# Optimization experiments

Hardware: AMD Instinct MI355X
Metric: run time of the kernel (lower is better)

The kernel has to match this reference:

```python
import jax, jax.numpy as jnp
import numpy as np

D_MODEL = 1024
NHEAD = 16
HEAD_DIM = D_MODEL // NHEAD
D_FF = 4096
B, S = 2, 2048
LN_EPS = 1e-5


def _linear_params(key, d_out, d_in):
    kw, kb = jax.random.split(key)
    lim = 1.0 / np.sqrt(d_in)
    W = jax.random.uniform(kw, (d_out, d_in), jnp.float32, -lim, lim)
    b = jax.random.uniform(kb, (d_out,), jnp.float32, -lim, lim)
    return W, b


def setup_inputs() -> dict:
    key = jax.random.key(0)
    ks = jax.random.split(key, 8)
    src = jax.random.normal(ks[0], (B, S, D_MODEL), jnp.float32)
    mask = jax.random.randint(ks[1], (B, S), 0, 2).astype(bool)
    Wq, bq = _linear_params(ks[2], D_MODEL, D_MODEL)
    Wk, bk = _linear_params(ks[3], D_MODEL, D_MODEL)
    Wv, bv = _linear_params(ks[4], D_MODEL, D_MODEL)
    Wo, bo = _linear_params(ks[5], D_MODEL, D_MODEL)
    W1, b1 = _linear_params(ks[6], D_FF, D_MODEL)
    W2, b2 = _linear_params(ks[7], D_MODEL, D_FF)
    ln1_g = jnp.ones((D_MODEL,), jnp.float32)
    ln1_b = jnp.zeros((D_MODEL,), jnp.float32)
    ln2_g = jnp.ones((D_MODEL,), jnp.float32)
    ln2_b = jnp.zeros((D_MODEL,), jnp.float32)
    return dict(src=src, mask=mask, Wq=Wq, bq=bq, Wk=Wk, bk=bk, Wv=Wv, bv=bv,
                Wo=Wo, bo=bo, W1=W1, b1=b1, W2=W2, b2=b2,
                ln1_g=ln1_g, ln1_b=ln1_b, ln2_g=ln2_g, ln2_b=ln2_b)


def _layernorm(x, g, b):
    mu = jnp.mean(x, axis=-1, keepdims=True)
    var = jnp.mean(jnp.square(x - mu), axis=-1, keepdims=True)
    return (x - mu) * jax.lax.rsqrt(var + LN_EPS) * g + b


def reference(src, mask, Wq, bq, Wk, bk, Wv, bv, Wo, bo, W1, b1, W2, b2,
              ln1_g, ln1_b, ln2_g, ln2_b):
    batch, seq, _ = src.shape
    src_norm = _layernorm(src, ln1_g, ln1_b)
    # projections (torch Linear: x @ W.T + b), split heads -> [B,H,S,Dh]
    def proj(W, b):
        y = jnp.einsum('bsi,oi->bso', src_norm, W) + b
        return y.reshape(batch, seq, NHEAD, HEAD_DIM).transpose(0, 2, 1, 3)
    q, k, v = proj(Wq, bq), proj(Wk, bk), proj(Wv, bv)
    scores = jnp.einsum('bhqd,bhkd->bhqk', q, k) / np.sqrt(HEAD_DIM)
    scores = jnp.where(mask[:, None, None, :], -10000.0, scores)
    attn_probs = jax.nn.softmax(scores, axis=-1)
    attn_out = jnp.einsum('bhqk,bhkd->bhqd', attn_probs, v)
    attn_out = attn_out.transpose(0, 2, 1, 3).reshape(batch, seq, D_MODEL)
    attn_out = jnp.einsum('bsi,oi->bso', attn_out, Wo) + bo
    src = src + attn_out
    src_norm2 = _layernorm(src, ln2_g, ln2_b)
    h = jax.nn.relu(jnp.einsum('bsi,oi->bso', src_norm2, W1) + b1)
    ff = jnp.einsum('bsi,oi->bso', h, W2) + b2
    src = src + ff
    return (src, attn_probs)
```

## Files before the change

### kernel.cpp

```cpp
#include <hip/hip_runtime.h>
#include <math.h>

typedef __bf16 bf16;
typedef __bf16 bf16x4 __attribute__((ext_vector_type(4)));
typedef __bf16 bf16x8 __attribute__((ext_vector_type(8)));
typedef float f32x4 __attribute__((ext_vector_type(4)));

__device__ __forceinline__ f32x4 mfma16(bf16x8 a, bf16x8 b, f32x4 c) {
  return __builtin_amdgcn_mfma_f32_16x16x32_bf16(a, b, c, 0, 0, 0);
}

__device__ __forceinline__ void gload_lds16(const void* g, void* l) {
  __builtin_amdgcn_global_load_lds((__attribute__((address_space(1))) void*)(g),
                                   (__attribute__((address_space(3))) void*)(l),
                                   16, 0, 0);
}

__global__ __launch_bounds__(256)
void cvt_all(const float* __restrict__ Wq, const float* __restrict__ Wk,
             const float* __restrict__ Wv, const float* __restrict__ Wo,
             const float* __restrict__ W1, const float* __restrict__ W2,
             const float* __restrict__ bq, const float* __restrict__ bk,
             const float* __restrict__ bv, bf16* __restrict__ wqkv,
             bf16* __restrict__ wob, bf16* __restrict__ w1b,
             bf16* __restrict__ w2b, float* __restrict__ bqkv) {
  const int i = blockIdx.x * 256 + threadIdx.x;
  if (i < 3145728) {
    float4 v;
    bf16* dst;
    size_t di;
    if (i < 262144) { v = ((const float4*)Wq)[i]; dst = wqkv; di = i; }
    else if (i < 524288) { v = ((const float4*)Wk)[i - 262144]; dst = wqkv; di = i; }
    else if (i < 786432) { v = ((const float4*)Wv)[i - 524288]; dst = wqkv; di = i; }
    else if (i < 1048576) { v = ((const float4*)Wo)[i - 786432]; dst = wob; di = i - 786432; }
    else if (i < 2097152) { v = ((const float4*)W1)[i - 1048576]; dst = w1b; di = i - 1048576; }
    else { v = ((const float4*)W2)[i - 2097152]; dst = w2b; di = i - 2097152; }
    bf16x4 o;
    o[0] = (bf16)v.x; o[1] = (bf16)v.y; o[2] = (bf16)v.z; o[3] = (bf16)v.w;
    reinterpret_cast<bf16x4*>(dst)[di] = o;
  } else {
    const int j = i - 3145728;
    const float* s = (j < 256) ? bq : ((j < 512) ? bk : bv);
    reinterpret_cast<float4*>(bqkv)[j] = reinterpret_cast<const float4*>(s)[j & 255];
  }
}

__global__ __launch_bounds__(256)
void ln_bf16(const float* __restrict__ x, const float* __restrict__ g,
             const float* __restrict__ bta, bf16* __restrict__ y) {
  const int row = blockIdx.x, t = threadIdx.x;
  const float4 v = reinterpret_cast<const float4*>(x)[(size_t)row * 256 + t];
  float s1 = v.x + v.y + v.z + v.w;
  float s2 = v.x * v.x + v.y * v.y + v.z * v.z + v.w * v.w;
#pragma unroll
  for (int m = 1; m < 64; m <<= 1) {
    s1 += __shfl_xor(s1, m);
    s2 += __shfl_xor(s2, m);
  }
  __shared__ float red[8];
  if ((t & 63) == 0) { red[(t >> 6) * 2] = s1; red[(t >> 6) * 2 + 1] = s2; }
  __syncthreads();
  s1 = red[0] + red[2] + red[4] + red[6];
  s2 = red[1] + red[3] + red[5] + red[7];
  const float mu = s1 * (1.f / 1024.f);
  const float rs = rsqrtf(s2 * (1.f / 1024.f) - mu * mu + 1e-5f);
  const float4 gv = reinterpret_cast<const float4*>(g)[t];
  const float4 bv = reinterpret_cast<const float4*>(bta)[t];
  bf16x4 o;
  o[0] = (bf16)((v.x - mu) * rs * gv.x + bv.x);
  o[1] = (bf16)((v.y - mu) * rs * gv.y + bv.y);
  o[2] = (bf16)((v.z - mu) * rs * gv.z + bv.z);
  o[3] = (bf16)((v.w - mu) * rs * gv.w + bv.w);
  reinterpret_cast<bf16x4*>(y)[(size_t)row * 256 + t] = o;
}

__global__ __launch_bounds__(256)
void tr_v(const bf16* __restrict__ QKV, bf16* __restrict__ VT) {
  __shared__ bf16 T[64 * 80];
  const int t = threadIdx.x;
  const int sb = blockIdx.x * 64, h = blockIdx.y, b = blockIdx.z;
  const int srow = t >> 2, c16 = t & 3;
  const bf16* src = QKV + (size_t)(b * 2048 + sb + srow) * 3072 + 2048 + h * 64 + c16 * 16;
  bf16x8 a0 = *reinterpret_cast<const bf16x8*>(src);
  bf16x8 a1 = *reinterpret_cast<const bf16x8*>(src + 8);
  *reinterpret_cast<bf16x8*>(&T[srow * 80 + c16 * 16]) = a0;
  *reinterpret_cast<bf16x8*>(&T[srow * 80 + c16 * 16 + 8]) = a1;
  __syncthreads();
  const int drow = t >> 2, sq = t & 3;
  bf16x8 o0, o1;
#pragma unroll
  for (int j = 0; j < 8; ++j) o0[j] = T[(sq * 16 + j) * 80 + drow];
#pragma unroll
  for (int j = 0; j < 8; ++j) o1[j] = T[(sq * 16 + 8 + j) * 80 + drow];
  bf16* dst = VT + ((size_t)(b * 16 + h) * 64 + drow) * 2048 + sb + sq * 16;
  *reinterpret_cast<bf16x8*>(dst) = o0;
  *reinterpret_cast<bf16x8*>(dst + 8) = o1;
}

template <bool OUT_BF16, bool RELU, bool RES, bool QSC>
__global__ __launch_bounds__(256)
void gemm_bt(const bf16* __restrict__ A, const bf16* __restrict__ Bw,
             const float* __restrict__ bias, const float* __restrict__ res,
             void* __restrict__ Cout, int M, int N, int K) {
  __shared__ bf16 As[3][128 * 32];
  __shared__ bf16 Bs[3][128 * 32];
  const int t = threadIdx.x, wave = t >> 6, lane = t & 63;
  const int l15 = lane & 15, lhi = lane >> 4;
  const int nwg = gridDim.x * gridDim.y;
  const int orig = blockIdx.y * gridDim.x + blockIdx.x;
  const int wgid = (orig & 7) * (nwg >> 3) + (orig >> 3);
  const int bx = wgid % gridDim.x, by = wgid / gridDim.x;
  const int m0 = by * 128, n0 = bx * 128;
  const int wm = (wave >> 1) * 64, wn = (wave & 1) * 64;
  const f32x4 z4 = {0.f, 0.f, 0.f, 0.f};
  f32x4 acc[4][4];
#pragma unroll
  for (int m = 0; m < 4; ++m)
#pragma unroll
    for (int n = 0; n < 4; ++n) acc[m][n] = z4;

  const int soff0 = wave * 1024 + lane * 16;
  const int soff1 = (4 + wave) * 1024 + lane * 16;
  const int srow0 = soff0 >> 6, scol0 = (soff0 & 63) >> 1;
  const int srow1 = soff1 >> 6, scol1 = (soff1 & 63) >> 1;

#define GEMM_STAGE(k0, bb)                                                    \
  do {                                                                        \
    gload_lds16(A + (size_t)(m0 + srow0) * K + (k0) + scol0,                  \
                (char*)As[bb] + soff0);                                       \
    gload_lds16(Bw + (size_t)(n0 + srow0) * K + (k0) + scol0,                 \
                (char*)Bs[bb] + soff0);                                       \
    gload_lds16(A + (size_t)(m0 + srow1) * K + (k0) + scol1,                  \
                (char*)As[bb] + soff1);                                       \
    gload_lds16(Bw + (size_t)(n0 + srow1) * K + (k0) + scol1,                 \
                (char*)Bs[bb] + soff1);                                       \
  } while (0)

  const int nt = K >> 5;
  GEMM_STAGE(0, 0);
  GEMM_STAGE(32, 1);
  asm volatile("s_waitcnt vmcnt(4)" ::: "memory");
  __builtin_amdgcn_s_barrier();

  for (int kt = 0; kt < nt; ++kt) {
    if (kt + 2 < nt) GEMM_STAGE((kt + 2) * 32, (kt + 2) % 3);
    const bf16* Ac = As[kt % 3];
    const bf16* Bc = Bs[kt % 3];
    bf16x8 af[4], bfr[4];
#pragma unroll
    for (int m = 0; m < 4; ++m)
      af[m] = *reinterpret_cast<const bf16x8*>(&Ac[(wm + m * 16 + l15) * 32 + lhi * 8]);
#pragma unroll
    for (int n = 0; n < 4; ++n)
      bfr[n] = *reinterpret_cast<const bf16x8*>(&Bc[(wn + n * 16 + l15) * 32 + lhi * 8]);
    __builtin_amdgcn_s_setprio(1);
#pragma unroll
    for (int m = 0; m < 4; ++m)
#pragma unroll
      for (int n = 0; n < 4; ++n) acc[m][n] = mfma16(af[m], bfr[n], acc[m][n]);
    __builtin_amdgcn_s_setprio(0);
    if (kt + 1 < nt) {
      if (kt + 2 < nt)
        asm volatile("s_waitcnt vmcnt(4)" ::: "memory");
      else
        asm volatile("s_waitcnt vmcnt(0)" ::: "memory");
      __builtin_amdgcn_s_barrier();
    }
  }
#undef GEMM_STAGE

  const float sc = (QSC && n0 < 1024) ? 0.125f : 1.0f;
#pragma unroll
  for (int m = 0; m < 4; ++m) {
    const int row_base = m0 + wm + m * 16 + lhi * 4;
#pragma unroll
    for (int n = 0; n < 4; ++n) {
      const int col = n0 + wn + n * 16 + l15;
      const float bv = bias[col];
#pragma unroll
      for (int r = 0; r < 4; ++r) {
        const int row = row_base + r;
        float v = (acc[m][n][r] + bv) * sc;
        if (RELU) v = v > 0.f ? v : 0.f;
        if (RES) v += res[(size_t)row * N + col];
        if (OUT_BF16)
          ((bf16*)Cout)[(size_t)row * N + col] = (bf16)v;
        else
          ((float*)Cout)[(size_t)row * N + col] = v;
      }
    }
  }
}

__global__ __launch_bounds__(512)
void attn_fused2(const bf16* __restrict__ Qp, const bf16* __restrict__ Kp,
                 const bf16* __restrict__ VTp, const int* __restrict__ mask,
                 float* __restrict__ probs, bf16* __restrict__ Ob) {
  constexpr int S = 2048, LD = 3072, KB = 128, NT = S / KB;
  __shared__ bf16 Kt[KB * 64];
  __shared__ bf16 Vt[64 * KB];
  __shared__ bf16 P[128 * KB];
  __shared__ float msk2[2][KB];
  const int t = threadIdx.x, wave = t >> 6, lane = t & 63;
  const int l15 = lane & 15, lhi = lane >> 4;
  const int flat = blockIdx.x + 16 * (blockIdx.y + 16 * blockIdx.z);
  const int wg = (flat & 7) * 64 + (flat >> 3);
  const int q0 = (wg & 15) * 128, h = (wg >> 4) & 15, b = wg >> 8;
  const int* mrow = mask + b * S;
  const f32x4 z4 = {0.f, 0.f, 0.f, 0.f};

  const bf16* kgp[2];
  const bf16* vgp[2];
  int soff[2];
#pragma unroll
  for (int i = 0; i < 2; ++i) {
    const int off = (i * 8 + wave) * 1024 + lane * 16;
    soff[i] = off;
    const int krow = off >> 7, kbin = off & 127;
    kgp[i] = Kp + (size_t)(b * S + krow) * LD + h * 64 + ((kbin ^ ((krow & 7) << 4)) >> 1);
    const int d = off >> 8, vbin = off & 255;
    vgp[i] = VTp + (size_t)((b * 16 + h) * 64 + d) * S + ((vbin ^ ((d & 7) << 4)) >> 1);
  }

  bf16x8 qf[2];
#pragma unroll
  for (int ks = 0; ks < 2; ++ks)
    qf[ks] = *reinterpret_cast<const bf16x8*>(
        Qp + (size_t)(b * S + q0 + wave * 16 + l15) * LD + h * 64 + ks * 32 + lhi * 8);

  bf16x8 kreg[2];
  float mnext;
#pragma unroll
  for (int i = 0; i < 2; ++i) kreg[i] = *reinterpret_cast<const bf16x8*>(kgp[i]);
  mnext = (t < KB) ? (mrow[t] ? 0.f : 1.f) : 0.f;
#pragma unroll
  for (int i = 0; i < 2; ++i)
    *reinterpret_cast<bf16x8*>((char*)Kt + soff[i]) = kreg[i];
  if (t < KB) msk2[0][t] = mnext;
  __syncthreads();

  float lpart = 0.f;
  for (int kt = 0; kt < NT; ++kt) {
    const int kv0 = kt * KB;
    if (kt + 1 < NT) {
#pragma unroll
      for (int i = 0; i < 2; ++i)
        kreg[i] = *reinterpret_cast<const bf16x8*>(kgp[i] + (size_t)(kv0 + KB) * LD);
      mnext = (t < KB) ? (mrow[kv0 + KB + t] ? 0.f : 1.f) : 0.f;
    }
    const char* kb = (kt & 1) ? (const char*)Vt : (const char*)Kt;
    const float* mc = msk2[kt & 1];
    f32x4 sa[8];
#pragma unroll
    for (int n = 0; n < 8; ++n) sa[n] = z4;
    __builtin_amdgcn_s_setprio(1);
#pragma unroll
    for (int ks = 0; ks < 2; ++ks)
#pragma unroll
      for (int n = 0; n < 8; ++n) {
        const int krow = n * 16 + l15;
        bf16x8 kf = *reinterpret_cast<const bf16x8*>(
            kb + krow * 128 + ((ks * 64 + lhi * 16) ^ ((krow & 7) << 4)));
        sa[n] = mfma16(kf, qf[ks], sa[n]);
      }
    __builtin_amdgcn_s_setprio(0);
#pragma unroll
    for (int n = 0; n < 8; ++n)
#pragma unroll
      for (int r = 0; r < 4; ++r)
        lpart += __expf(sa[n][r] - 15.f) * mc[n * 16 + lhi * 4 + r];
    if (kt + 1 < NT) {
      char* kbn = ((kt + 1) & 1) ? (char*)Vt : (char*)Kt;
#pragma unroll
      for (int i = 0; i < 2; ++i)
        *reinterpret_cast<bf16x8*>(kbn + soff[i]) = kreg[i];
      if (t < KB) msk2[(kt + 1) & 1][t] = mnext;
    }
    __syncthreads();
  }
  lpart += __shfl_xor(lpart, 16);
  lpart += __shfl_xor(lpart, 32);
  const float il = 1.f / lpart;

  f32x4 oa[4];
#pragma unroll
  for (int n = 0; n < 4; ++n) oa[n] = z4;
  float* pbase = probs + ((size_t)(b * 16 + h) * S + q0 + wave * 16 + l15) * S;
  const int prw = wave * 16 + l15;

  bf16x8 vreg[2];
#pragma unroll
  for (int i = 0; i < 2; ++i) {
    kreg[i] = *reinterpret_cast<const bf16x8*>(kgp[i]);
    vreg[i] = *reinterpret_cast<const bf16x8*>(vgp[i]);
  }
  mnext = (t < KB) ? (mrow[t] ? 0.f : 1.f) : 0.f;
#pragma unroll
  for (int i = 0; i < 2; ++i) {
    *reinterpret_cast<bf16x8*>((char*)Kt + soff[i]) = kreg[i];
    *reinterpret_cast<bf16x8*>((char*)Vt + soff[i]) = vreg[i];
  }
  if (t < KB) msk2[0][t] = mnext;
  __syncthreads();

  for (int kt = 0; kt < NT; ++kt) {
    const int kv0 = kt * KB;
    if (kt + 1 < NT) {
#pragma unroll
      for (int i = 0; i < 2; ++i) {
        kreg[i] = *reinterpret_cast<const bf16x8*>(kgp[i] + (size_t)(kv0 + KB) * LD);
        vreg[i] = *reinterpret_cast<const bf16x8*>(vgp[i] + kv0 + KB);
      }
      mnext = (t < KB) ? (mrow[kv0 + KB + t] ? 0.f : 1.f) : 0.f;
    }

    f32x4 sa[8];
#pragma unroll
    for (int n = 0; n < 8; ++n) sa[n] = z4;
    __builtin_amdgcn_s_setprio(1);
#pragma unroll
    for (int ks = 0; ks < 2; ++ks)
#pragma unroll
      for (int n = 0; n < 8; ++n) {
        const int krow = n * 16 + l15;
        bf16x8 kf = *reinterpret_cast<const bf16x8*>(
            (char*)Kt + krow * 128 + ((ks * 64 + lhi * 16) ^ ((krow & 7) << 4)));
        sa[n] = mfma16(kf, qf[ks], sa[n]);
      }
    __builtin_amdgcn_s_setprio(0);

#pragma unroll
    for (int n = 0; n < 8; ++n) {
      f32x4 pn;
#pragma unroll
      for (int r = 0; r < 4; ++r)
        pn[r] = __expf(sa[n][r] - 15.f) * msk2[0][n * 16 + lhi * 4 + r] * il;
      *reinterpret_cast<f32x4*>(pbase + kv0 + n * 16 + lhi * 4) = pn;
      bf16x4 pb;
      pb[0] = (bf16)pn[0]; pb[1] = (bf16)pn[1];
      pb[2] = (bf16)pn[2]; pb[3] = (bf16)pn[3];
      *reinterpret_cast<bf16x4*>(
          (char*)P + prw * 256 + ((n * 32 + lhi * 8) ^ ((prw & 7) << 4))) = pb;
    }
    __builtin_amdgcn_s_setprio(1);
#pragma unroll
    for (int ks = 0; ks < 4; ++ks) {
      bf16x8 pf = *reinterpret_cast<const bf16x8*>(
          (char*)P + prw * 256 + ((ks * 64 + lhi * 16) ^ ((prw & 7) << 4)));
#pragma unroll
      for (int nn = 0; nn < 4; ++nn) {
        const int vr = nn * 16 + l15;
        bf16x8 vf = *reinterpret_cast<const bf16x8*>(
            (char*)Vt + vr * 256 + ((ks * 64 + lhi * 16) ^ ((vr & 7) << 4)));
        oa[nn] = mfma16(pf, vf, oa[nn]);
      }
    }
    __builtin_amdgcn_s_setprio(0);
    __syncthreads();
    if (kt + 1 < NT) {
#pragma unroll
      for (int i = 0; i < 2; ++i) {
        *reinterpret_cast<bf16x8*>((char*)Kt + soff[i]) = kreg[i];
        *reinterpret_cast<bf16x8*>((char*)Vt + soff[i]) = vreg[i];
      }
      if (t < KB) msk2[0][t] = mnext;
    }
    __syncthreads();
  }

#pragma unroll
  for (int nn = 0; nn < 4; ++nn)
#pragma unroll
    for (int r = 0; r < 4; ++r)
      Ob[(size_t)(b * S + q0 + wave * 16 + lhi * 4 + r) * 1024 + h * 64 + nn * 16 + l15] =
          (bf16)oa[nn][r];
}

extern "C" void kernel_launch(void* const* d_in, const int* in_sizes, int n_in,
                              void* d_out, int out_size, void* d_ws, size_t ws_size,
                              hipStream_t stream) {
  const float* src = (const float*)d_in[0];
  const int* mask = (const int*)d_in[1];
  const float* Wq = (const float*)d_in[2];
  const float* bq = (const float*)d_in[3];
  const float* Wk = (const float*)d_in[4];
  const float* bk = (const float*)d_in[5];
  const float* Wv = (const float*)d_in[6];
  const float* bv = (const float*)d_in[7];
  const float* Wo = (const float*)d_in[8];
  const float* bo = (const float*)d_in[9];
  const float* W1 = (const float*)d_in[10];
  const float* b1 = (const float*)d_in[11];
  const float* W2 = (const float*)d_in[12];
  const float* b2 = (const float*)d_in[13];
  const float* ln1g = (const float*)d_in[14];
  const float* ln1b = (const float*)d_in[15];
  const float* ln2g = (const float*)d_in[16];
  const float* ln2b = (const float*)d_in[17];

  float* out0 = (float*)d_out;
  float* probs = (float*)d_out + (size_t)4194304;

  char* w = (char*)d_ws;
  const size_t MB = 1u << 20;
  bf16* wqkv = (bf16*)(w);
  bf16* wob = (bf16*)(w + 6 * MB);
  bf16* w1b = (bf16*)(w + 8 * MB);
  bf16* w2b = (bf16*)(w + 16 * MB);
  bf16* xn = (bf16*)(w + 24 * MB);
  bf16* QKV = (bf16*)(w + 32 * MB);
  bf16* Ob = (bf16*)(w + 56 * MB);
  bf16* hb = (bf16*)(w + 32 * MB);
  bf16* VT = (bf16*)(w + 64 * MB);
  float* s2 = (float*)(w + 64 * MB);
  float* bqkv = (float*)(w + 80 * MB);

  cvt_all<<<12291, 256, 0, stream>>>(Wq, Wk, Wv, Wo, W1, W2, bq, bk, bv,
                                     wqkv, wob, w1b, w2b, bqkv);

  ln_bf16<<<4096, 256, 0, stream>>>(src, ln1g, ln1b, xn);
  gemm_bt<true, false, false, true><<<dim3(24, 32), 256, 0, stream>>>(
      xn, wqkv, bqkv, nullptr, QKV, 4096, 3072, 1024);
  tr_v<<<dim3(32, 16, 2), 256, 0, stream>>>(QKV, VT);
  attn_fused2<<<dim3(16, 16, 2), 512, 0, stream>>>(
      QKV, QKV + 1024, VT, mask, probs, Ob);
  gemm_bt<false, false, true, false><<<dim3(8, 32), 256, 0, stream>>>(
      Ob, wob, bo, src, s2, 4096, 1024, 1024);
  ln_bf16<<<4096, 256, 0, stream>>>(s2, ln2g, ln2b, xn);
  gemm_bt<true, true, false, false><<<dim3(32, 32), 256, 0, stream>>>(
      xn, w1b, b1, nullptr, hb, 4096, 4096, 1024);
  gemm_bt<false, false, true, false><<<dim3(8, 32), 256, 0, stream>>>(
      hb, w2b, b2, s2, out0, 4096, 1024, 4096);

  (void)in_sizes; (void)n_in; (void)out_size; (void)ws_size;
}
```

Baseline: 434.8 us.

## Use 64-row tiles for N=1024 GEMMs, exp2 softmax, nontemporal probs stores

Templates the GEMM on M-tile size and launches the two N=1024 GEMMs with 64-row tiles, doubling their workgroup count so more CUs are busy. Folds log2(e) into the Q scale so attention uses exp2 without the constant shift. Defers the 1/l normalization of the output to the epilogue instead of applying it per probability before the PV product. Writes the probability matrix with nontemporal stores to reduce cache pollution. Dropping the -15 shift may risk overflow for large scores.

```diff
diff --git a/kernel.cpp b/kernel.cpp
--- a/kernel.cpp
+++ b/kernel.cpp
@@ -97,12 +97,14 @@
   *reinterpret_cast<bf16x8*>(dst + 8) = o1;
 }
 
-template <bool OUT_BF16, bool RELU, bool RES, bool QSC>
+template <int TM, bool OUT_BF16, bool RELU, bool RES, bool QSC>
 __global__ __launch_bounds__(256)
 void gemm_bt(const bf16* __restrict__ A, const bf16* __restrict__ Bw,
              const float* __restrict__ bias, const float* __restrict__ res,
              void* __restrict__ Cout, int M, int N, int K) {
-  __shared__ bf16 As[3][128 * 32];
+  constexpr int MR = TM / 32;
+  constexpr int ACH = TM / 64;
+  __shared__ bf16 As[3][TM * 32];
   __shared__ bf16 Bs[3][128 * 32];
   const int t = threadIdx.x, wave = t >> 6, lane = t & 63;
   const int l15 = lane & 15, lhi = lane >> 4;
@@ -110,68 +112,78 @@
   const int orig = blockIdx.y * gridDim.x + blockIdx.x;
   const int wgid = (orig & 7) * (nwg >> 3) + (orig >> 3);
   const int bx = wgid % gridDim.x, by = wgid / gridDim.x;
-  const int m0 = by * 128, n0 = bx * 128;
-  const int wm = (wave >> 1) * 64, wn = (wave & 1) * 64;
+  const int m0 = by * TM, n0 = bx * 128;
+  const int wm = (wave >> 1) * (TM / 2), wn = (wave & 1) * 64;
   const f32x4 z4 = {0.f, 0.f, 0.f, 0.f};
-  f32x4 acc[4][4];
-#pragma unroll
-  for (int m = 0; m < 4; ++m)
+  f32x4 acc[MR][4];
+#pragma unroll
+  for (int m = 0; m < MR; ++m)
 #pragma unroll
     for (int n = 0; n < 4; ++n) acc[m][n] = z4;
 
-  const int soff0 = wave * 1024 + lane * 16;
-  const int soff1 = (4 + wave) * 1024 + lane * 16;
-  const int srow0 = soff0 >> 6, scol0 = (soff0 & 63) >> 1;
-  const int srow1 = soff1 >> 6, scol1 = (soff1 & 63) >> 1;
+  int soff[2], srow[2], scol[2];
+#pragma unroll
+  for (int i = 0; i < 2; ++i) {
+    soff[i] = (i * 4 + wave) * 1024 + lane * 16;
+    srow[i] = soff[i] >> 6;
+    scol[i] = (soff[i] & 63) >> 1;
+  }
 
 #define GEMM_STAGE(k0, bb)                                                    \
   do {                                                                        \
-    gload_lds16(A + (size_t)(m0 + srow0) * K + (k0) + scol0,                  \
-                (char*)As[bb] + soff0);                                       \
-    gload_lds16(Bw + (size_t)(n0 + srow0) * K + (k0) + scol0,                 \
-                (char*)Bs[bb] + soff0);                                       \
-    gload_lds16(A + (size_t)(m0 + srow1) * K + (k0) + scol1,                  \
-                (char*)As[bb] + soff1);                                       \
-    gload_lds16(Bw + (size_t)(n0 + srow1) * K + (k0) + scol1,                 \
-                (char*)Bs[bb] + soff1);                                       \
+    _Pragma("unroll")                                                         \
+    for (int i = 0; i < ACH; ++i)                                             \
+      gload_lds16(A + (size_t)(m0 + srow[i]) * K + (k0) + scol[i],            \
+                  (char*)As[bb] + soff[i]);                                   \
+    _Pragma("unroll")                                                         \
+    for (int i = 0; i < 2; ++i)                                               \
+      gload_lds16(Bw + (size_t)(n0 + srow[i]) * K + (k0) + scol[i],           \
+                  (char*)Bs[bb] + soff[i]);                                   \
   } while (0)
 
   const int nt = K >> 5;
   GEMM_STAGE(0, 0);
   GEMM_STAGE(32, 1);
-  asm volatile("s_waitcnt vmcnt(4)" ::: "memory");
+  if constexpr (TM == 128)
+    asm volatile("s_waitcnt vmcnt(4)" ::: "memory");
+  else
+    asm volatile("s_waitcnt vmcnt(3)" ::: "memory");
   __builtin_amdgcn_s_barrier();
 
   for (int kt = 0; kt < nt; ++kt) {
     if (kt + 2 < nt) GEMM_STAGE((kt + 2) * 32, (kt + 2) % 3);
     const bf16* Ac = As[kt % 3];
     const bf16* Bc = Bs[kt % 3];
-    bf16x8 af[4], bfr[4];
-#pragma unroll
-    for (int m = 0; m < 4; ++m)
+    bf16x8 af[MR], bfr[4];
+#pragma unroll
+    for (int m = 0; m < MR; ++m)
       af[m] = *reinterpret_cast<const bf16x8*>(&Ac[(wm + m * 16 + l15) * 32 + lhi * 8]);
 #pragma unroll
     for (int n = 0; n < 4; ++n)
       bfr[n] = *reinterpret_cast<const bf16x8*>(&Bc[(wn + n * 16 + l15) * 32 + lhi * 8]);
     __builtin_amdgcn_s_setprio(1);
 #pragma unroll
-    for (int m = 0; m < 4; ++m)
+    for (int m = 0; m < MR; ++m)
 #pragma unroll
       for (int n = 0; n < 4; ++n) acc[m][n] = mfma16(af[m], bfr[n], acc[m][n]);
     __builtin_amdgcn_s_setprio(0);
     if (kt + 1 < nt) {
-      if (kt + 2 < nt)
-        asm volatile("s_waitcnt vmcnt(4)" ::: "memory");
-      else
+      if (kt + 2 < nt) {
+        if constexpr (TM == 128)
+          asm volatile("s_waitcnt vmcnt(4)" ::: "memory");
+        else
+          asm volatile("s_waitcnt vmcnt(3)" ::: "memory");
+      } else {
         asm volatile("s_waitcnt vmcnt(0)" ::: "memory");
+      }
       __builtin_amdgcn_s_barrier();
     }
   }
 #undef GEMM_STAGE
 
-  const float sc = (QSC && n0 < 1024) ? 0.125f : 1.0f;
-#pragma unroll
-  for (int m = 0; m < 4; ++m) {
+  const float sc = (QSC && n0 < 1024) ? 0.18033688011112042f : 1.0f;
+#pragma unroll
+  for (int m = 0; m < MR; ++m) {
     const int row_base = m0 + wm + m * 16 + lhi * 4;
 #pragma unroll
     for (int n = 0; n < 4; ++n) {
@@ -268,7 +280,7 @@
     for (int n = 0; n < 8; ++n)
 #pragma unroll
       for (int r = 0; r < 4; ++r)
-        lpart += __expf(sa[n][r] - 15.f) * mc[n * 16 + lhi * 4 + r];
+        lpart += __builtin_exp2f(sa[n][r]) * mc[n * 16 + lhi * 4 + r];
     if (kt + 1 < NT) {
       char* kbn = ((kt + 1) & 1) ? (char*)Vt : (char*)Kt;
 #pragma unroll
@@ -331,14 +343,16 @@
 
 #pragma unroll
     for (int n = 0; n < 8; ++n) {
-      f32x4 pn;
-#pragma unroll
-      for (int r = 0; r < 4; ++r)
-        pn[r] = __expf(sa[n][r] - 15.f) * msk2[0][n * 16 + lhi * 4 + r] * il;
-      *reinterpret_cast<f32x4*>(pbase + kv0 + n * 16 + lhi * 4) = pn;
+      f32x4 praw, pn;
+#pragma unroll
+      for (int r = 0; r < 4; ++r) {
+        praw[r] = __builtin_exp2f(sa[n][r]) * msk2[0][n * 16 + lhi * 4 + r];
+        pn[r] = praw[r] * il;
+      }
+      __builtin_nontemporal_store(pn, reinterpret_cast<f32x4*>(pbase + kv0 + n * 16 + lhi * 4));
       bf16x4 pb;
-      pb[0] = (bf16)pn[0]; pb[1] = (bf16)pn[1];
-      pb[2] = (bf16)pn[2]; pb[3] = (bf16)pn[3];
+      pb[0] = (bf16)praw[0]; pb[1] = (bf16)praw[1];
+      pb[2] = (bf16)praw[2]; pb[3] = (bf16)praw[3];
       *reinterpret_cast<bf16x4*>(
           (char*)P + prw * 256 + ((n * 32 + lhi * 8) ^ ((prw & 7) << 4))) = pb;
     }
@@ -368,12 +382,15 @@
     __syncthreads();
   }
 
+  float il4[4];
+#pragma unroll
+  for (int r = 0; r < 4; ++r) il4[r] = __shfl(il, lhi * 4 + r);
 #pragma unroll
   for (int nn = 0; nn < 4; ++nn)
 #pragma unroll
     for (int r = 0; r < 4; ++r)
       Ob[(size_t)(b * S + q0 + wave * 16 + lhi * 4 + r) * 1024 + h * 64 + nn * 16 + l15] =
-          (bf16)oa[nn][r];
+          (bf16)(oa[nn][r] * il4[r]);
 }
 
 extern "C" void kernel_launch(void* const* d_in, const int* in_sizes, int n_in,
@@ -419,17 +436,17 @@
                                      wqkv, wob, w1b, w2b, bqkv);
 
   ln_bf16<<<4096, 256, 0, stream>>>(src, ln1g, ln1b, xn);
-  gemm_bt<true, false, false, true><<<dim3(24, 32), 256, 0, stream>>>(
+  gemm_bt<128, true, false, false, true><<<dim3(24, 32), 256, 0, stream>>>(
       xn, wqkv, bqkv, nullptr, QKV, 4096, 3072, 1024);
   tr_v<<<dim3(32, 16, 2), 256, 0, stream>>>(QKV, VT);
   attn_fused2<<<dim3(16, 16, 2), 512, 0, stream>>>(
       QKV, QKV + 1024, VT, mask, probs, Ob);
-  gemm_bt<false, false, true, false><<<dim3(8, 32), 256, 0, stream>>>(
+  gemm_bt<64, false, false, true, false><<<dim3(8, 64), 256, 0, stream>>>(
       Ob, wob, bo, src, s2, 4096, 1024, 1024);
   ln_bf16<<<4096, 256, 0, stream>>>(s2, ln2g, ln2b, xn);
-  gemm_bt<true, true, false, false><<<dim3(32, 32), 256, 0, stream>>>(
+  gemm_bt<128, true, true, false, false><<<dim3(32, 32), 256, 0, stream>>>(
       xn, w1b, b1, nullptr, hb, 4096, 4096, 1024);
-  gemm_bt<false, false, true, false><<<dim3(8, 32), 256, 0, stream>>>(
+  gemm_bt<64, false, false, true, false><<<dim3(8, 64), 256, 0, stream>>>(
       hb, w2b, b2, s2, out0, 4096, 1024, 4096);
 
   (void)in_sizes; (void)n_in; (void)out_size; (void)ws_size;
```

Result: faster. 424.4 us (-2.4%).
